# Kernel tuning notes

Hardware: AMD Instinct MI355X
Metric: run time of the kernel (lower is better)

Reference implementation:

```python
import jax, jax.numpy as jnp
import numpy as np

B, S, D, H, DFF = 4, 2048, 768, 12, 3072
DK = D // H

def setup_inputs() -> dict:
    key = jax.random.key(0)
    ks = jax.random.split(key, 16)
    sc = 0.02
    inp = {
        'src': jax.random.normal(ks[0], (B, S, D), jnp.float32),
        'mask': jnp.ones((B, 1, 1, S), jnp.int32),
        'Wq': jax.random.normal(ks[1], (D, D), jnp.float32) * sc,
        'bq': jnp.zeros((D,), jnp.float32),
        'Wk': jax.random.normal(ks[2], (D, D), jnp.float32) * sc,
        'bk': jnp.zeros((D,), jnp.float32),
        'Wv': jax.random.normal(ks[3], (D, D), jnp.float32) * sc,
        'bv': jnp.zeros((D,), jnp.float32),
        'Wo': jax.random.normal(ks[4], (D, D), jnp.float32) * sc,
        'bo': jnp.zeros((D,), jnp.float32),
        'W1': jax.random.normal(ks[5], (D, DFF), jnp.float32) * sc,
        'b1': jnp.zeros((DFF,), jnp.float32),
        'W2': jax.random.normal(ks[6], (DFF, D), jnp.float32) * sc,
        'b2': jnp.zeros((D,), jnp.float32),
        'ln1_g': jnp.ones((D,), jnp.float32), 'ln1_b': jnp.zeros((D,), jnp.float32),
        'ln2_g': jnp.ones((D,), jnp.float32), 'ln2_b': jnp.zeros((D,), jnp.float32),
    }
    return inp

def _layernorm(x, g, b, eps=1e-5):
    mu = jnp.mean(x, axis=-1, keepdims=True)
    var = jnp.mean(jnp.square(x - mu), axis=-1, keepdims=True)
    return (x - mu) * jax.lax.rsqrt(var + eps) * g + b

def reference(src, mask, Wq, bq, Wk, bk, Wv, bv, Wo, bo, W1, b1, W2, b2, ln1_g, ln1_b, ln2_g, ln2_b):
    # Multi-head self-attention (dropout in eval mode -> identity)
    q = (src @ Wq + bq).reshape(B, S, H, DK).transpose(0, 2, 1, 3)  # [B,H,S,dk]
    k = (src @ Wk + bk).reshape(B, S, H, DK).transpose(0, 2, 1, 3)
    v = (src @ Wv + bv).reshape(B, S, H, DK).transpose(0, 2, 1, 3)
    scores = jnp.einsum('bhqd,bhkd->bhqk', q, k) / jnp.sqrt(jnp.float32(DK))
    scores = jnp.where(mask == 0, jnp.float32(-1e9), scores)
    attn = jax.nn.softmax(scores, axis=-1)
    ctx = jnp.einsum('bhqk,bhkd->bhqd', attn, v)  # [B,H,S,dk]
    ctx = ctx.transpose(0, 2, 1, 3).reshape(B, S, D)
    attn_out = ctx @ Wo + bo
    x = _layernorm(src + attn_out, ln1_g, ln1_b)
    ffn = jax.nn.relu(x @ W1 + b1) @ W2 + b2
    return _layernorm(x + ffn, ln2_g, ln2_b)
```

## Files before the change

### kernel.cpp

```cpp
#include <hip/hip_runtime.h>
#include <hip/hip_bf16.h>
#include <stdint.h>

constexpr int BB = 4;
constexpr int SS = 2048;
constexpr int DD = 768;
constexpr int HH = 12;
constexpr int DKK = 64;
constexpr int DFF2 = 3072;
constexpr int MR = BB * SS;

typedef __attribute__((ext_vector_type(4))) short short4v;
typedef __attribute__((ext_vector_type(8))) short short8v;
typedef __attribute__((ext_vector_type(4))) float f32x4;
typedef __attribute__((ext_vector_type(16))) float f32x16;
typedef __attribute__((ext_vector_type(4))) float float4v;
typedef __attribute__((ext_vector_type(4))) unsigned int u32x4;

static __device__ inline short f2bs(float f) {
    __hip_bfloat16 h = __float2bfloat16(f);
    return (short)__builtin_bit_cast(unsigned short, h);
}
static __device__ inline float bs2f(short s) {
    __hip_bfloat16 h = __builtin_bit_cast(__hip_bfloat16, (unsigned short)s);
    return __bfloat162float(h);
}

static __device__ inline void glds16(const void* g, void* l) {
    __builtin_amdgcn_global_load_lds(
        (const __attribute__((address_space(1))) void*)g,
        (__attribute__((address_space(3))) void*)l, 16, 0, 0);
}

static __device__ inline unsigned cvtpk(float a, float b) {
    unsigned d;
    asm("v_cvt_pk_bf16_f32 %0, %1, %2" : "=v"(d) : "v"(a), "v"(b));
    return d;
}
static __device__ inline short8v pk4(unsigned a, unsigned b, unsigned c, unsigned d) {
    u32x4 w; w[0] = a; w[1] = b; w[2] = c; w[3] = d;
    return __builtin_bit_cast(short8v, w);
}

__global__ __launch_bounds__(256) void cast_f32_bf16(const float* __restrict__ in,
                                                     short* __restrict__ out, int n) {
    int i = (blockIdx.x * 256 + threadIdx.x) * 4;
    if (i < n) {
        float4v v = *(const float4v*)&in[i];
        short4v o;
        o[0] = f2bs(v[0]); o[1] = f2bs(v[1]); o[2] = f2bs(v[2]); o[3] = f2bs(v[3]);
        *(short4v*)&out[i] = o;
    }
}

__global__ __launch_bounds__(256) void transpose_cast(const float* __restrict__ W,
                                                      short* __restrict__ Wt, int K, int N) {
    __shared__ float tile[32][33];
    int n0 = blockIdx.x * 32, k0 = blockIdx.y * 32;
    int tx = threadIdx.x & 31, ty = threadIdx.x >> 5;
    #pragma unroll
    for (int i = 0; i < 32; i += 8)
        tile[ty + i][tx] = W[(size_t)(k0 + ty + i) * N + n0 + tx];
    __syncthreads();
    #pragma unroll
    for (int i = 0; i < 32; i += 8)
        Wt[(size_t)(n0 + ty + i) * K + k0 + tx] = f2bs(tile[tx][ty + i]);
}

__global__ __launch_bounds__(256) void vtrans(const short* __restrict__ V,
                                              short* __restrict__ Vt) {
    __shared__ short t[64][72];
    const int tid = threadIdx.x;
    const size_t base = (size_t)blockIdx.y * SS * DKK;
    const int s0 = blockIdx.x * 64;
    int r = tid >> 3, c = (tid & 7) * 8;
    #pragma unroll
    for (int it = 0; it < 2; it++)
        *(short8v*)&t[it * 32 + r][c] =
            *(const short8v*)&V[base + (size_t)(s0 + it * 32 + r) * DKK + c];
    __syncthreads();
    int d = tid >> 2, grp = (tid & 3) * 16;
    short8v o0, o1;
    #pragma unroll
    for (int e = 0; e < 8; e++) {
        int p0 = e, p1 = 8 + e;
        o0[e] = t[grp + (p0 & 3) + 8 * ((p0 >> 2) & 1) + 4 * (p0 >> 3)][d];
        o1[e] = t[grp + (p1 & 3) + 8 * ((p1 >> 2) & 1) + 4 * (p1 >> 3)][d];
    }
    int c0 = 2 * (tid & 3), c1 = c0 + 1;
    int p0 = c0 ^ (d & 7), p1 = c1 ^ (d & 7);
    *(short8v*)&Vt[base + (size_t)d * SS + s0 + p0 * 8] = o0;
    *(short8v*)&Vt[base + (size_t)d * SS + s0 + p1 * 8] = o1;
}

template <int EPI>
__global__ __launch_bounds__(256) void gemm_bt(
    const short* __restrict__ A, const short* __restrict__ Bt,
    int Nn, int Kn,
    const float* __restrict__ bias0, const float* __restrict__ bias1,
    const float* __restrict__ bias2,
    short* __restrict__ out0, short* __restrict__ out1, short* __restrict__ out2) {
    __shared__ alignas(16) short sA[2][128 * 32];
    __shared__ alignas(16) short sB[2][128 * 32];
    const int tid = threadIdx.x;
    const int wave = tid >> 6, lane = tid & 63;
    const int g = lane >> 4, qq = lane & 15;
    const int wm = (wave >> 1) * 64, wn = (wave & 1) * 64;

    const int gx = gridDim.x;
    const int nwg = gx * gridDim.y;
    const int wgid = blockIdx.y * gx + blockIdx.x;
    const int cpx = nwg >> 3;
    const int swz = (wgid & 7) * cpx + (wgid >> 3);
    const int bx = swz % gx, by = swz / gx;
    const int m0 = by * 128, n0 = bx * 128;

    const int e0 = wave * 512 + lane * 8;
    const int r0 = e0 >> 5, c0 = e0 & 31;

    const f32x4 zero = {0.0f, 0.0f, 0.0f, 0.0f};
    f32x4 acc[4][4];
    #pragma unroll
    for (int i = 0; i < 4; i++)
        #pragma unroll
        for (int j = 0; j < 4; j++) acc[i][j] = zero;

    const int NK = Kn >> 5;
    glds16(&A[(size_t)(m0 + r0) * Kn + c0], &sA[0][wave * 512]);
    glds16(&A[(size_t)(m0 + r0 + 64) * Kn + c0], &sA[0][wave * 512 + 2048]);
    glds16(&Bt[(size_t)(n0 + r0) * Kn + c0], &sB[0][wave * 512]);
    glds16(&Bt[(size_t)(n0 + r0 + 64) * Kn + c0], &sB[0][wave * 512 + 2048]);
    __syncthreads();

    for (int kt = 0; kt < NK; ++kt) {
        const int cur = kt & 1;
        if (kt + 1 < NK) {
            const int k1 = (kt + 1) * 32;
            glds16(&A[(size_t)(m0 + r0) * Kn + k1 + c0], &sA[cur ^ 1][wave * 512]);
            glds16(&A[(size_t)(m0 + r0 + 64) * Kn + k1 + c0], &sA[cur ^ 1][wave * 512 + 2048]);
            glds16(&Bt[(size_t)(n0 + r0) * Kn + k1 + c0], &sB[cur ^ 1][wave * 512]);
            glds16(&Bt[(size_t)(n0 + r0 + 64) * Kn + k1 + c0], &sB[cur ^ 1][wave * 512 + 2048]);
        }
        short8v af[4], bf[4];
        #pragma unroll
        for (int i = 0; i < 4; i++) {
            af[i] = *(const short8v*)&sA[cur][(wm + i * 16 + qq) * 32 + 8 * g];
            bf[i] = *(const short8v*)&sB[cur][(wn + i * 16 + qq) * 32 + 8 * g];
        }
        #pragma unroll
        for (int i = 0; i < 4; i++)
            #pragma unroll
            for (int j = 0; j < 4; j++)
                acc[i][j] = __builtin_amdgcn_mfma_f32_16x16x32_bf16(af[i], bf[j], acc[i][j], 0, 0, 0);
        __syncthreads();
    }

    if (EPI == 2) {
        int which = bx / 6;
        const float* bias = (which == 0) ? bias0 : ((which == 1) ? bias1 : bias2);
        short* outp = (which == 0) ? out0 : ((which == 1) ? out1 : out2);
        float scale = (which == 0) ? 0.125f * 1.44269504088896f : 1.0f;
        #pragma unroll
        for (int i = 0; i < 4; i++)
            #pragma unroll
            for (int j = 0; j < 4; j++)
                #pragma unroll
                for (int r = 0; r < 4; r++) {
                    int row = m0 + wm + i * 16 + g * 4 + r;
                    int col = n0 - which * DD + wn + j * 16 + qq;
                    float vv = (acc[i][j][r] + bias[col]) * scale;
                    int b_ = row >> 11, s_ = row & 2047;
                    int h_ = col >> 6, d_ = col & 63;
                    if (which == 1)
                        d_ = (((d_ >> 3) ^ (s_ & 7)) << 3) | (d_ & 7);
                    outp[(((size_t)(b_ * HH + h_)) * SS + s_) * DKK + d_] = f2bs(vv);
                }
    } else {
        #pragma unroll
        for (int i = 0; i < 4; i++)
            #pragma unroll
            for (int j = 0; j < 4; j++)
                #pragma unroll
                for (int r = 0; r < 4; r++) {
                    int row = m0 + wm + i * 16 + g * 4 + r;
                    int col = n0 + wn + j * 16 + qq;
                    float vv = acc[i][j][r] + bias0[col];
                    if (EPI == 1) vv = fmaxf(vv, 0.0f);
                    out0[(size_t)row * Nn + col] = f2bs(vv);
                }
    }
}

__global__ __launch_bounds__(256) void attn_kernel(
    const short* __restrict__ Q, const short* __restrict__ Kb,
    const short* __restrict__ Vt, const int* __restrict__ mask,
    short* __restrict__ ctx) {
    __shared__ alignas(16) short sK[2][64 * 64];
    __shared__ alignas(16) short sV[2][64 * 64];
    __shared__ float sAl[4][32];
    __shared__ unsigned char smask[256];
    const int tid = threadIdx.x;
    const int wave = tid >> 6, lane = tid & 63;
    const int hi = lane >> 5, ln = lane & 31;
    constexpr int NT = SS / 64;

    int flat = blockIdx.y * gridDim.x + blockIdx.x;
    int nw = (flat & 7) * 96 + (flat >> 3);
    const int bh = nw >> 4, qb = nw & 15;
    const int b_ = bh / HH, h_ = bh % HH;
    const int q0 = qb * 128 + wave * 32;
    const size_t base = (size_t)bh * SS * DKK;

    {
        const int* mp = mask + b_ * SS + tid * 8;
        unsigned char by = 0;
        #pragma unroll
        for (int e = 0; e < 8; e++) by |= (unsigned char)((mp[e] != 0) << e);
        smask[tid] = by;
    }

    short8v qf[4];
    {
        const short* qp = &Q[base + (size_t)(q0 + ln) * DKK];
        #pragma unroll
        for (int c = 0; c < 4; c++)
            qf[c] = *(const short8v*)(qp + 16 * c + 8 * hi);
    }

    f32x16 O0, O1;
    #pragma unroll
    for (int r = 0; r < 16; r++) { O0[r] = 0.0f; O1[r] = 0.0f; }
    float lreg = 0.0f;

    const int stgrow = wave * 8 + (lane >> 3);
    const int stgc = (lane & 7) * 8;

    const int rsz = (ln & 7) << 4;

    glds16(&Kb[base + (size_t)stgrow * DKK + stgc], &sK[0][wave * 512]);
    glds16(&Kb[base + (size_t)(stgrow + 32) * DKK + stgc], &sK[0][2048 + wave * 512]);
    glds16(&Vt[base + (size_t)stgrow * SS + stgc], &sV[0][wave * 512]);
    glds16(&Vt[base + (size_t)(stgrow + 32) * SS + stgc], &sV[0][2048 + wave * 512]);
    __syncthreads();

    for (int t = 0; t < NT; ++t) {
        const int kv0 = t * 64;
        const int cur = t & 1;
        if (t + 1 < NT) {
            const int kn = kv0 + 64;
            glds16(&Kb[base + (size_t)(kn + stgrow) * DKK + stgc], &sK[cur ^ 1][wave * 512]);
            glds16(&Kb[base + (size_t)(kn + stgrow + 32) * DKK + stgc], &sK[cur ^ 1][2048 + wave * 512]);
            glds16(&Vt[base + (size_t)stgrow * SS + kn + stgc], &sV[cur ^ 1][wave * 512]);
            glds16(&Vt[base + (size_t)(stgrow + 32) * SS + kn + stgc], &sV[cur ^ 1][2048 + wave * 512]);
        }
        const char* kr0 = (const char*)&sK[cur][0] + ln * 128;
        const char* kr1 = kr0 + 32 * 128;
        const char* vr0 = (const char*)&sV[cur][0] + ln * 128;
        const char* vr1 = vr0 + 32 * 128;

        f32x16 s0, s1;
        #pragma unroll
        for (int r = 0; r < 16; r++) { s0[r] = 0.0f; s1[r] = 0.0f; }
        __builtin_amdgcn_s_setprio(1);
        #pragma unroll
        for (int c = 0; c < 4; c++) {
            int off = (32 * c + 16 * hi) ^ rsz;
            s0 = __builtin_amdgcn_mfma_f32_32x32x16_bf16(
                *(const short8v*)(kr0 + off), qf[c], s0, 0, 0, 0);
            s1 = __builtin_amdgcn_mfma_f32_32x32x16_bf16(
                *(const short8v*)(kr1 + off), qf[c], s1, 0, 0, 0);
        }
        __builtin_amdgcn_s_setprio(0);

        uint64_t mb = *(const uint64_t*)&smask[kv0 >> 3];
        if (mb != ~0ull) {
            #pragma unroll
            for (int r = 0; r < 16; r++) {
                int kvr = (r & 3) + 8 * (r >> 2) + 4 * hi;
                if (!((mb >> kvr) & 1)) s0[r] = -1.5e9f;
                if (!((mb >> (kvr + 32)) & 1)) s1[r] = -1.5e9f;
            }
        }

        float ps = 0.0f;
        unsigned w0[8], w1[8];
        #pragma unroll
        for (int r8 = 0; r8 < 8; ++r8) {
            float a0 = __builtin_amdgcn_exp2f(s0[2 * r8]);
            float a1 = __builtin_amdgcn_exp2f(s0[2 * r8 + 1]);
            ps += a0 + a1;
            w0[r8] = cvtpk(a0, a1);
            float b0 = __builtin_amdgcn_exp2f(s1[2 * r8]);
            float b1 = __builtin_amdgcn_exp2f(s1[2 * r8 + 1]);
            ps += b0 + b1;
            w1[r8] = cvtpk(b0, b1);
        }
        lreg += ps;

        short8v p00 = pk4(w0[0], w0[1], w0[2], w0[3]);
        short8v p01 = pk4(w0[4], w0[5], w0[6], w0[7]);
        short8v p10 = pk4(w1[0], w1[1], w1[2], w1[3]);
        short8v p11 = pk4(w1[4], w1[5], w1[6], w1[7]);

        __builtin_amdgcn_s_setprio(1);
        #pragma unroll
        for (int cc = 0; cc < 4; cc++) {
            int off = (32 * cc + 16 * hi) ^ rsz;
            short8v pa = (cc == 0) ? p00 : (cc == 1) ? p01 : (cc == 2) ? p10 : p11;
            O0 = __builtin_amdgcn_mfma_f32_32x32x16_bf16(
                pa, *(const short8v*)(vr0 + off), O0, 0, 0, 0);
            O1 = __builtin_amdgcn_mfma_f32_32x32x16_bf16(
                pa, *(const short8v*)(vr1 + off), O1, 0, 0, 0);
        }
        __builtin_amdgcn_s_setprio(0);
        __syncthreads();
    }

    lreg += __shfl_xor(lreg, 32);
    sAl[wave][ln] = 1.0f / lreg;
    #pragma unroll
    for (int r = 0; r < 16; r++) {
        int rho = (r & 3) + 8 * (r >> 2) + 4 * hi;
        float li = sAl[wave][rho];
        size_t rowoff = (size_t)(b_ * SS + q0 + rho) * DD + h_ * DKK;
        ctx[rowoff + ln] = f2bs(O0[r] * li);
        ctx[rowoff + 32 + ln] = f2bs(O1[r] * li);
    }
}

template <int WB, int WF>
__global__ __launch_bounds__(256) void ln_fused(
    const float* __restrict__ in1, const short* __restrict__ in2,
    const float* __restrict__ gw, const float* __restrict__ bw,
    short* __restrict__ outb, float* __restrict__ outf) {
    const int row = blockIdx.x;
    const int tid = threadIdx.x;
    float4v v = {0.0f, 0.0f, 0.0f, 0.0f};
    if (tid < 192) {
        float4v a = *(const float4v*)&in1[(size_t)row * DD + tid * 4];
        short4v b = *(const short4v*)&in2[(size_t)row * DD + tid * 4];
        #pragma unroll
        for (int e = 0; e < 4; e++) v[e] = a[e] + bs2f(b[e]);
    }
    float s = v[0] + v[1] + v[2] + v[3];
    float s2 = v[0] * v[0] + v[1] * v[1] + v[2] * v[2] + v[3] * v[3];
    #pragma unroll
    for (int off = 1; off < 64; off <<= 1) {
        s += __shfl_xor(s, off);
        s2 += __shfl_xor(s2, off);
    }
    __shared__ float red[8];
    int wv = tid >> 6;
    if ((tid & 63) == 0) { red[wv] = s; red[4 + wv] = s2; }
    __syncthreads();
    s = red[0] + red[1] + red[2] + red[3];
    s2 = red[4] + red[5] + red[6] + red[7];
    float mu = s / DD;
    float var = s2 / DD - mu * mu;
    float rs = rsqrtf(var + 1e-5f);
    if (tid < 192) {
        float4v gv = *(const float4v*)&gw[tid * 4];
        float4v bv = *(const float4v*)&bw[tid * 4];
        float4v y;
        #pragma unroll
        for (int e = 0; e < 4; e++) y[e] = (v[e] - mu) * rs * gv[e] + bv[e];
        if (WB) {
            short4v o;
            #pragma unroll
            for (int e = 0; e < 4; e++) o[e] = f2bs(y[e]);
            *(short4v*)&outb[(size_t)row * DD + tid * 4] = o;
        }
        if (WF) *(float4v*)&outf[(size_t)row * DD + tid * 4] = y;
    }
}

extern "C" void kernel_launch(void* const* d_in, const int* in_sizes, int n_in,
                              void* d_out, int out_size, void* d_ws, size_t ws_size,
                              hipStream_t stream) {
    (void)in_sizes; (void)n_in; (void)out_size; (void)ws_size;
    const float* src = (const float*)d_in[0];
    const int* mask = (const int*)d_in[1];
    const float* Wq = (const float*)d_in[2];
    const float* bq = (const float*)d_in[3];
    const float* Wk = (const float*)d_in[4];
    const float* bk = (const float*)d_in[5];
    const float* Wv = (const float*)d_in[6];
    const float* bv = (const float*)d_in[7];
    const float* Wo = (const float*)d_in[8];
    const float* bo = (const float*)d_in[9];
    const float* W1 = (const float*)d_in[10];
    const float* b1 = (const float*)d_in[11];
    const float* W2 = (const float*)d_in[12];
    const float* b2 = (const float*)d_in[13];
    const float* ln1_g = (const float*)d_in[14];
    const float* ln1_b = (const float*)d_in[15];
    const float* ln2_g = (const float*)d_in[16];
    const float* ln2_b = (const float*)d_in[17];

    char* ws = (char*)d_ws;
    const size_t SB = (size_t)MR * DD * 2;
    short* src_b  = (short*)(ws);
    short* Wqkv_t = (short*)(ws + SB);
    short* qb     = (short*)(ws + SB + 3538944);
    short* kb_    = qb + (size_t)MR * DD;
    short* vb_    = kb_ + (size_t)MR * DD;
    short* ctxb   = vb_ + (size_t)MR * DD;
    short* hb     = qb;
    short* Wo_t   = (short*)(ws + SB + 3538944 + 4 * SB);
    short* x_b    = (short*)(ws + SB + 3538944 + 4 * SB + 1179648);
    short* W1_t   = (short*)((char*)x_b + SB);
    short* W2_t   = (short*)((char*)W1_t + 4718592);
    float* x_f    = (float*)((char*)W2_t + 4718592);
    short* vt_    = x_b;
    short* attn_b = src_b;
    short* ffn_b  = src_b;

    cast_f32_bf16<<<(MR * DD) / 1024, 256, 0, stream>>>(src, src_b, MR * DD);
    transpose_cast<<<dim3(24, 24), 256, 0, stream>>>(Wq, Wqkv_t, DD, DD);
    transpose_cast<<<dim3(24, 24), 256, 0, stream>>>(Wk, Wqkv_t + DD * DD, DD, DD);
    transpose_cast<<<dim3(24, 24), 256, 0, stream>>>(Wv, Wqkv_t + 2 * DD * DD, DD, DD);
    transpose_cast<<<dim3(24, 24), 256, 0, stream>>>(Wo, Wo_t, DD, DD);
    transpose_cast<<<dim3(96, 24), 256, 0, stream>>>(W1, W1_t, DD, DFF2);
    transpose_cast<<<dim3(24, 96), 256, 0, stream>>>(W2, W2_t, DFF2, DD);

    gemm_bt<2><<<dim3(2304 / 128, MR / 128), 256, 0, stream>>>(
        src_b, Wqkv_t, 2304, DD, bq, bk, bv, qb, kb_, vb_);

    vtrans<<<dim3(SS / 64, BB * HH), 256, 0, stream>>>(vb_, vt_);

    attn_kernel<<<dim3(SS / 128, BB * HH), 256, 0, stream>>>(qb, kb_, vt_, mask, ctxb);

    gemm_bt<0><<<dim3(DD / 128, MR / 128), 256, 0, stream>>>(
        ctxb, Wo_t, DD, DD, bo, nullptr, nullptr, attn_b, nullptr, nullptr);

    ln_fused<1, 1><<<MR, 256, 0, stream>>>(src, attn_b, ln1_g, ln1_b, x_b, x_f);

    gemm_bt<1><<<dim3(DFF2 / 128, MR / 128), 256, 0, stream>>>(
        x_b, W1_t, DFF2, DD, b1, nullptr, nullptr, hb, nullptr, nullptr);
    gemm_bt<0><<<dim3(DD / 128, MR / 128), 256, 0, stream>>>(
        hb, W2_t, DD, DFF2, b2, nullptr, nullptr, ffn_b, nullptr, nullptr);

    ln_fused<0, 1><<<MR, 256, 0, stream>>>(x_f, ffn_b, ln2_g, ln2_b, nullptr, (float*)d_out);
}
```

Measured before the change: 326.5 us.

## Triple-buffer LDS tiles in GEMM and attention with one partial-wait barrier

```diff
diff --git a/kernel.cpp b/kernel.cpp
--- a/kernel.cpp
+++ b/kernel.cpp
@@ -40,6 +40,19 @@
 static __device__ inline short8v pk4(unsigned a, unsigned b, unsigned c, unsigned d) {
     u32x4 w; w[0] = a; w[1] = b; w[2] = c; w[3] = d;
     return __builtin_bit_cast(short8v, w);
+}
+
+static __device__ inline void bar_vmcnt4() {
+    __builtin_amdgcn_sched_barrier(0);
+    asm volatile("s_waitcnt vmcnt(4)" ::: "memory");
+    __builtin_amdgcn_s_barrier();
+    __builtin_amdgcn_sched_barrier(0);
+}
+static __device__ inline void bar_vmcnt0() {
+    __builtin_amdgcn_sched_barrier(0);
+    asm volatile("s_waitcnt vmcnt(0)" ::: "memory");
+    __builtin_amdgcn_s_barrier();
+    __builtin_amdgcn_sched_barrier(0);
 }
 
 __global__ __launch_bounds__(256) void cast_f32_bf16(const float* __restrict__ in,
@@ -100,8 +113,8 @@
     const float* __restrict__ bias0, const float* __restrict__ bias1,
     const float* __restrict__ bias2,
     short* __restrict__ out0, short* __restrict__ out1, short* __restrict__ out2) {
-    __shared__ alignas(16) short sA[2][128 * 32];
-    __shared__ alignas(16) short sB[2][128 * 32];
+    __shared__ alignas(16) short sA[3][128 * 32];
+    __shared__ alignas(16) short sB[3][128 * 32];
     const int tid = threadIdx.x;
     const int wave = tid >> 6, lane = tid & 63;
     const int g = lane >> 4, qq = lane & 15;
@@ -132,14 +145,17 @@
     glds16(&Bt[(size_t)(n0 + r0 + 64) * Kn + c0], &sB[0][wave * 512 + 2048]);
     __syncthreads();
 
+    int cur = 0, nxt = 1;
     for (int kt = 0; kt < NK; ++kt) {
-        const int cur = kt & 1;
         if (kt + 1 < NK) {
             const int k1 = (kt + 1) * 32;
-            glds16(&A[(size_t)(m0 + r0) * Kn + k1 + c0], &sA[cur ^ 1][wave * 512]);
-            glds16(&A[(size_t)(m0 + r0 + 64) * Kn + k1 + c0], &sA[cur ^ 1][wave * 512 + 2048]);
-            glds16(&Bt[(size_t)(n0 + r0) * Kn + k1 + c0], &sB[cur ^ 1][wave * 512]);
-            glds16(&Bt[(size_t)(n0 + r0 + 64) * Kn + k1 + c0], &sB[cur ^ 1][wave * 512 + 2048]);
+            glds16(&A[(size_t)(m0 + r0) * Kn + k1 + c0], &sA[nxt][wave * 512]);
+            glds16(&A[(size_t)(m0 + r0 + 64) * Kn + k1 + c0], &sA[nxt][wave * 512 + 2048]);
+            glds16(&Bt[(size_t)(n0 + r0) * Kn + k1 + c0], &sB[nxt][wave * 512]);
+            glds16(&Bt[(size_t)(n0 + r0 + 64) * Kn + k1 + c0], &sB[nxt][wave * 512 + 2048]);
+            bar_vmcnt4();
+        } else {
+            bar_vmcnt0();
         }
         short8v af[4], bf[4];
         #pragma unroll
@@ -152,7 +168,8 @@
             #pragma unroll
             for (int j = 0; j < 4; j++)
                 acc[i][j] = __builtin_amdgcn_mfma_f32_16x16x32_bf16(af[i], bf[j], acc[i][j], 0, 0, 0);
-        __syncthreads();
+        cur = nxt;
+        nxt = (nxt == 2) ? 0 : nxt + 1;
     }
 
     if (EPI == 2) {
@@ -195,8 +212,8 @@
     const short* __restrict__ Q, const short* __restrict__ Kb,
     const short* __restrict__ Vt, const int* __restrict__ mask,
     short* __restrict__ ctx) {
-    __shared__ alignas(16) short sK[2][64 * 64];
-    __shared__ alignas(16) short sV[2][64 * 64];
+    __shared__ alignas(16) short sK[3][64 * 64];
+    __shared__ alignas(16) short sV[3][64 * 64];
     __shared__ float sAl[4][32];
     __shared__ unsigned char smask[256];
     const int tid = threadIdx.x;
@@ -234,7 +251,6 @@
 
     const int stgrow = wave * 8 + (lane >> 3);
     const int stgc = (lane & 7) * 8;
-
     const int rsz = (ln & 7) << 4;
 
     glds16(&Kb[base + (size_t)stgrow * DKK + stgc], &sK[0][wave * 512]);
@@ -243,15 +259,18 @@
     glds16(&Vt[base + (size_t)(stgrow + 32) * SS + stgc], &sV[0][2048 + wave * 512]);
     __syncthreads();
 
+    int cur = 0, nxt = 1;
     for (int t = 0; t < NT; ++t) {
         const int kv0 = t * 64;
-        const int cur = t & 1;
         if (t + 1 < NT) {
             const int kn = kv0 + 64;
-            glds16(&Kb[base + (size_t)(kn + stgrow) * DKK + stgc], &sK[cur ^ 1][wave * 512]);
-            glds16(&Kb[base + (size_t)(kn + stgrow + 32) * DKK + stgc], &sK[cur ^ 1][2048 + wave * 512]);
-            glds16(&Vt[base + (size_t)stgrow * SS + kn + stgc], &sV[cur ^ 1][wave * 512]);
-            glds16(&Vt[base + (size_t)(stgrow + 32) * SS + kn + stgc], &sV[cur ^ 1][2048 + wave * 512]);
+            glds16(&Kb[base + (size_t)(kn + stgrow) * DKK + stgc], &sK[nxt][wave * 512]);
+            glds16(&Kb[base + (size_t)(kn + stgrow + 32) * DKK + stgc], &sK[nxt][2048 + wave * 512]);
+            glds16(&Vt[base + (size_t)stgrow * SS + kn + stgc], &sV[nxt][wave * 512]);
+            glds16(&Vt[base + (size_t)(stgrow + 32) * SS + kn + stgc], &sV[nxt][2048 + wave * 512]);
+            bar_vmcnt4();
+        } else {
+            bar_vmcnt0();
         }
         const char* kr0 = (const char*)&sK[cur][0] + ln * 128;
         const char* kr1 = kr0 + 32 * 128;
@@ -313,7 +332,8 @@
                 pa, *(const short8v*)(vr1 + off), O1, 0, 0, 0);
         }
         __builtin_amdgcn_s_setprio(0);
-        __syncthreads();
+        cur = nxt;
+        nxt = (nxt == 2) ? 0 : nxt + 1;
     }
 
     lreg += __shfl_xor(lreg, 32);
```

Result: faster. 318.0 us (-2.6%).
